# Kernel tuning notes

Measured on AMD Instinct MI355X. Metric: run time of the kernel, lower is better.

## Reference

```python
import jax, jax.numpy as jnp
import numpy as np

ITER = 6
GAMMA = 0.99
Q = 0.95


def _maxpool(x, win, stride, pad):
    # NCHW max pool
    return jax.lax.reduce_window(
        x, -jnp.inf, jax.lax.max,
        (1, 1, win, win), (1, 1, stride, stride),
        ((0, 0), (0, 0), (pad, pad), (pad, pad)))


def _nearest(x, size):
    # torch F.interpolate(mode='nearest'): src = floor(dst * in / out)
    H, W = size
    h_in, w_in = x.shape[2], x.shape[3]
    ih = (jnp.arange(H) * h_in) // H
    iw = (jnp.arange(W) * w_in) // W
    return x[:, :, ih[:, None], iw[None, :]]


def setup_inputs() -> dict:
    key = jax.random.key(0)
    ks = jax.random.split(key, 4)
    C, mid = 256, 16  # mid = int(sqrt(C))
    x = jax.random.normal(ks[0], (16, C, 128, 128), jnp.float32)
    w1 = jax.random.normal(ks[1], (mid, C), jnp.float32) / np.sqrt(C)
    b1 = jnp.zeros((mid,), jnp.float32)
    w2 = jax.random.normal(ks[2], (C, mid), jnp.float32) / np.sqrt(mid)
    b2 = jnp.zeros((C,), jnp.float32)
    return {"x": x, "w1": w1, "b1": b1, "w2": w2, "b2": b2}


def reference(x, w1, b1, w2, b2):
    B, C, H, W = x.shape
    # --- quantile activation mask (detached) ---
    flat = x.reshape(B, C, H * W)
    thr = jnp.quantile(flat, Q, axis=-1)[:, :, None, None]  # [B,C,1,1]
    M = jax.lax.stop_gradient((x >= thr).astype(x.dtype))
    # --- propagate field ---
    feat = x * M
    out = feat
    for i in range(ITER):
        g = jnp.asarray(GAMMA ** (2 ** i), x.dtype)
        if i == 0:
            feat = _maxpool(feat, 3, 1, 1) * g  # same-resolution 3x3 pool
            out = jnp.maximum(out, feat)
        else:
            # 5x5 stride-2 pool -> scale -> nearest upsample back to (H,W)
            feat = _nearest(_maxpool(feat, 5, 2, 2) * g, (H, W))
            out = jnp.maximum(out, feat)
    # --- receptor modulator: 1x1 conv -> relu -> 1x1 conv -> sigmoid ---
    h = jax.nn.relu(jnp.einsum('bchw,mc->bmhw', out, w1) + b1[None, :, None, None])
    R = jax.nn.sigmoid(jnp.einsum('bmhw,cm->bchw', h, w2) + b2[None, :, None, None])
    y = x * R
    return y
```

## Files before the change

kernel.cpp:

```cpp
#include <hip/hip_runtime.h>
#include <cmath>
#include <cfloat>

#define HW_ 16384

__device__ __forceinline__ unsigned f2key(float f){
    unsigned u = __float_as_uint(f);
    return u ^ ((u & 0x80000000u) ? 0xFFFFFFFFu : 0x80000000u);
}
__device__ __forceinline__ float key2f(unsigned k){
    unsigned u = (k & 0x80000000u) ? (k ^ 0x80000000u) : ~k;
    return __uint_as_float(u);
}
__device__ __forceinline__ unsigned short f2bf(float f){
    unsigned u = __float_as_uint(f);
    unsigned r = u + 0x7FFFu + ((u >> 16) & 1u);
    return (unsigned short)(r >> 16);
}
__device__ __forceinline__ float bf2f(unsigned short s){
    return __uint_as_float((unsigned)s << 16);
}
__device__ __forceinline__ unsigned pkmax(unsigned a, unsigned b){
    unsigned d;
    asm("v_pk_max_u16 %0, %1, %2" : "=v"(d) : "v"(a), "v"(b));
    return d;
}
__device__ __forceinline__ unsigned alignb(unsigned hi, unsigned lo){
    unsigned d;
    asm("v_alignbit_b32 %0, %1, %2, 16" : "=v"(d) : "v"(hi), "v"(lo));
    return d;
}
__device__ __forceinline__ unsigned cvtpk(float lo, float hi){
    unsigned d;
    asm("v_cvt_pk_bf16_f32 %0, %1, %2" : "=v"(d) : "v"(lo), "v"(hi));
    return d;
}
__device__ __forceinline__ unsigned wscan_incl(unsigned v, int lane){
    #pragma unroll
    for (int o = 1; o < 64; o <<= 1){
        unsigned u = __shfl_up(v, o);
        v += (lane >= o) ? u : 0u;
    }
    return v;
}

typedef short bf16x8 __attribute__((ext_vector_type(8)));
typedef float f32x4  __attribute__((ext_vector_type(4)));
__device__ __forceinline__ bf16x8 tofrag(uint4 q){
    union { uint4 q; bf16x8 f; } u; u.q = q; return u.f;
}

__global__ __launch_bounds__(256) void k0_split(
    const float* __restrict__ w1, const float* __restrict__ w2,
    unsigned short* __restrict__ W1h, unsigned short* __restrict__ W1l,
    unsigned short* __restrict__ W2h, unsigned short* __restrict__ W2l)
{
    int e = blockIdx.x * 256 + threadIdx.x;
    if (e < 4096){
        float f = w1[e];
        unsigned short hi = f2bf(f);
        W1h[e] = hi;
        W1l[e] = f2bf(f - bf2f(hi));
    } else {
        int e2 = e - 4096;
        float f = w2[e2];
        unsigned short hi = f2bf(f);
        W2h[e2] = hi;
        W2l[e2] = f2bf(f - bf2f(hi));
    }
}

__global__ __launch_bounds__(512, 6) void k1f(
    const float* __restrict__ x,
    unsigned short* __restrict__ outp, unsigned short* __restrict__ m64g,
    float g1, float q2, float q3, float q4, float q5, float q6)
{
    __shared__ __align__(16) unsigned short C0[16384];
    __shared__ __align__(16) unsigned short H5s[8192];
    __shared__ unsigned hist[1024];
    __shared__ unsigned wsum[8];
    __shared__ unsigned redA[8], redB[8];
    __shared__ unsigned s_dA, s_dB, s_cloA, s_cloB, s_keyA, s_keyB;

    const int tid = threadIdx.x;
    const int lane = tid & 63;
    const int wid = tid >> 6;
    const unsigned bc = blockIdx.x;
    const float4* xp4 = (const float4*)(x + (size_t)bc * HW_);

    unsigned key[32];

    #pragma unroll
    for (int k = 0; k < 2; ++k) hist[tid + k * 512] = 0u;
    __syncthreads();
    #pragma unroll
    for (int k = 0; k < 8; ++k){
        float4 v = xp4[tid + k * 512];
        key[4*k+0] = f2key(v.x);
        key[4*k+1] = f2key(v.y);
        key[4*k+2] = f2key(v.z);
        key[4*k+3] = f2key(v.w);
        atomicAdd(&hist[key[4*k+0] >> 22], 1u);
        atomicAdd(&hist[key[4*k+1] >> 22], 1u);
        atomicAdd(&hist[key[4*k+2] >> 22], 1u);
        atomicAdd(&hist[key[4*k+3] >> 22], 1u);
    }
    __syncthreads();

    unsigned rA = 15563u, rB = 15564u;
    unsigned prefVal = 0u, prefMask = 0u;
    bool done = false;

    {
        unsigned part = hist[tid*2] + hist[tid*2+1];
        unsigned incl = wscan_incl(part, lane);
        if (lane == 63) wsum[wid] = incl;
        __syncthreads();
        unsigned off = 0;
        #pragma unroll
        for (int w = 0; w < 8; ++w) off += (w < wid) ? wsum[w] : 0u;
        unsigned phi = incl + off;
        unsigned plo = phi - part;
        if (rA >= plo && rA < phi){
            unsigned c = plo;
            #pragma unroll
            for (int k = 0; k < 2; ++k){
                unsigned hh = hist[tid*2+k];
                if (rA < c + hh){ s_dA = tid*2+k; s_cloA = c; break; }
                c += hh;
            }
        }
        if (rB >= plo && rB < phi){
            unsigned c = plo;
            #pragma unroll
            for (int k = 0; k < 2; ++k){
                unsigned hh = hist[tid*2+k];
                if (rB < c + hh){ s_dB = tid*2+k; s_cloB = c; break; }
                c += hh;
            }
        }
        __syncthreads();
        unsigned dA = s_dA, dB = s_dB;
        if (dA != dB){
            unsigned locA = 0u, locB = 0xFFFFFFFFu;
            #pragma unroll
            for (int e = 0; e < 32; ++e){
                unsigned d = key[e] >> 22;
                if (d == dA) locA = max(locA, key[e]);
                if (d == dB) locB = min(locB, key[e]);
            }
            #pragma unroll
            for (int o = 32; o > 0; o >>= 1){
                locA = max(locA, __shfl_down(locA, o));
                locB = min(locB, __shfl_down(locB, o));
            }
            if (lane == 0){ redA[wid] = locA; redB[wid] = locB; }
            __syncthreads();
            if (tid == 0){
                unsigned a = redA[0], b = redB[0];
                for (int w = 1; w < 8; ++w){ a = max(a, redA[w]); b = min(b, redB[w]); }
                s_keyA = a; s_keyB = b;
            }
            __syncthreads();
            done = true;
        } else {
            prefVal = dA << 22; prefMask = 0x3FFu << 22;
            rA -= s_cloA; rB -= s_cloB;
            __syncthreads();
        }
    }

    if (!done){
        const int shifts[3] = {14, 6, 0};
        const int bitsv[3]  = {8, 8, 6};
        for (int lvl = 0; lvl < 3 && !done; ++lvl){
            int shift = shifts[lvl];
            unsigned nb = 1u << bitsv[lvl];
            unsigned msk = nb - 1u;
            if (tid < (int)nb) hist[tid] = 0u;
            __syncthreads();
            #pragma unroll
            for (int e = 0; e < 32; ++e){
                if ((key[e] & prefMask) == prefVal)
                    atomicAdd(&hist[(key[e] >> shift) & msk], 1u);
            }
            __syncthreads();
            unsigned part = (tid < (int)nb) ? hist[tid] : 0u;
            unsigned incl = wscan_incl(part, lane);
            if (lane == 63) wsum[wid] = incl;
            __syncthreads();
            unsigned off = 0;
            #pragma unroll
            for (int w = 0; w < 8; ++w) off += (w < wid) ? wsum[w] : 0u;
            unsigned phi = incl + off;
            unsigned plo = phi - part;
            if (tid < (int)nb){
                if (rA >= plo && rA < phi){ s_dA = tid; s_cloA = plo; }
                if (rB >= plo && rB < phi){ s_dB = tid; s_cloB = plo; }
            }
            __syncthreads();
            unsigned dA = s_dA, dB = s_dB;
            if (dA != dB){
                unsigned mA = prefMask | (msk << shift);
                unsigned vAp = prefVal | (dA << shift);
                unsigned vBp = prefVal | (dB << shift);
                unsigned locA = 0u, locB = 0xFFFFFFFFu;
                #pragma unroll
                for (int e = 0; e < 32; ++e){
                    if ((key[e] & mA) == vAp) locA = max(locA, key[e]);
                    if ((key[e] & mA) == vBp) locB = min(locB, key[e]);
                }
                #pragma unroll
                for (int o = 32; o > 0; o >>= 1){
                    locA = max(locA, __shfl_down(locA, o));
                    locB = min(locB, __shfl_down(locB, o));
                }
                if (lane == 0){ redA[wid] = locA; redB[wid] = locB; }
                __syncthreads();
                if (tid == 0){
                    unsigned a = redA[0], b = redB[0];
                    for (int w = 1; w < 8; ++w){ a = max(a, redA[w]); b = min(b, redB[w]); }
                    s_keyA = a; s_keyB = b;
                }
                __syncthreads();
                done = true;
            } else {
                prefVal |= dA << shift;
                prefMask |= msk << shift;
                rA -= s_cloA; rB -= s_cloB;
                if (lvl == 2){
                    if (tid == 0){ s_keyA = prefVal; s_keyB = prefVal; }
                    done = true;
                }
                __syncthreads();
            }
        }
    }

    float vlo = key2f(s_keyA);
    float vhi = key2f(s_keyB);
    float idxq = 0.95f * 16383.0f;
    float frac = idxq - floorf(idxq);
    const float thr = vlo * (1.0f - frac) + vhi * frac;

    #pragma unroll
    for (int k = 0; k < 8; ++k){
        int i = tid + k * 512;
        float f0 = key2f(key[4*k+0]); f0 = (f0 >= thr) ? f0 : 0.0f;
        float f1 = key2f(key[4*k+1]); f1 = (f1 >= thr) ? f1 : 0.0f;
        float f2 = key2f(key[4*k+2]); f2 = (f2 >= thr) ? f2 : 0.0f;
        float f3 = key2f(key[4*k+3]); f3 = (f3 >= thr) ? f3 : 0.0f;
        uint2 w; w.x = cvtpk(f0, f1); w.y = cvtpk(f2, f3);
        ((uint2*)C0)[i] = w;
    }
    __syncthreads();

    {
        const unsigned* C0w = (const unsigned*)C0;
        unsigned* outp32 = (unsigned*)(outp + (size_t)bc * HW_);
        const int wc = lane;
        const int r0 = wid * 16;

        unsigned hmA, hmB, hmC, cB, cC;
        {
            int r = r0 - 1;
            if (r < 0){ hmA = 0u; }
            else {
                unsigned w = C0w[r*64 + wc];
                unsigned wl = __shfl_up(w, 1);
                unsigned wr = __shfl_down(w, 1);
                if (wc == 0)  wl = 0u;
                if (wc == 63) wr = 0u;
                hmA = pkmax(pkmax(alignb(w, wl), w), alignb(wr, w));
            }
        }
        {
            int r = r0;
            unsigned w = C0w[r*64 + wc];
            unsigned wl = __shfl_up(w, 1);
            unsigned wr = __shfl_down(w, 1);
            if (wc == 0)  wl = 0u;
            if (wc == 63) wr = 0u;
            hmB = pkmax(pkmax(alignb(w, wl), w), alignb(wr, w));
            cB = w;
        }
        #pragma unroll
        for (int rr = 0; rr < 16; ++rr){
            int r = r0 + rr;
            {
                int rn = r + 1;
                if (rn > 127){ hmC = 0u; cC = 0u; }
                else {
                    unsigned w = C0w[rn*64 + wc];
                    unsigned wl = __shfl_up(w, 1);
                    unsigned wr = __shfl_down(w, 1);
                    if (wc == 0)  wl = 0u;
                    if (wc == 63) wr = 0u;
                    hmC = pkmax(pkmax(alignb(w, wl), w), alignb(wr, w));
                    cC = w;
                }
            }
            unsigned p1 = pkmax(pkmax(hmA, hmB), hmC);
            float a0 = g1 * bf2f((unsigned short)(p1 & 0xFFFFu));
            float a1v = g1 * bf2f((unsigned short)(p1 >> 16));
            outp32[r*64 + wc] = pkmax(cB, cvtpk(a0, a1v));
            unsigned wjm1 = __shfl_up(p1, 1);
            unsigned wjp1 = __shfl_down(p1, 1);
            if (wc == 0)  wjm1 = 0u;
            if (wc == 63) wjp1 = 0u;
            unsigned s = pkmax(wjm1, p1);
            s = pkmax(s, s >> 16);
            s = pkmax(s, wjp1 & 0xFFFFu);
            H5s[r*64 + wc] = (unsigned short)s;
            hmA = hmB; hmB = hmC; cB = cC;
        }
    }
    __syncthreads();

    unsigned* U = (unsigned*)C0;
    unsigned* T = ((unsigned*)C0) + 2048;
    float mf[8];
    #pragma unroll
    for (int k = 0; k < 4; ++k){
        int q = tid + k * 512;
        int i = q >> 5, wj = q & 31;
        int rr = 2 * i;
        const unsigned* H5w = (const unsigned*)H5s;
        unsigned m = pkmax(H5w[rr*32 + wj], H5w[(rr+1)*32 + wj]);
        if (rr >= 1) m = pkmax(m, H5w[(rr-1)*32 + wj]);
        if (rr >= 2) m = pkmax(m, H5w[(rr-2)*32 + wj]);
        if (rr + 2 <= 127) m = pkmax(m, H5w[(rr+2)*32 + wj]);
        U[q] = m;
        mf[2*k]   = q2 * bf2f((unsigned short)(m & 0xFFFFu));
        mf[2*k+1] = q2 * bf2f((unsigned short)(m >> 16));
    }
    __syncthreads();

    const float gs[4] = {q3, q4, q5, q6};
    #pragma unroll
    for (int it = 0; it < 4; ++it){
        #pragma unroll
        for (int k = 0; k < 4; ++k){
            int q = tid + k * 512;
            unsigned w = U[q];
            unsigned wl = __shfl_up(w, 1);
            unsigned wr = __shfl_down(w, 1);
            if ((q & 31) == 0)  wl = 0u;
            if ((q & 31) == 31) wr = 0u;
            T[q] = pkmax(pkmax(alignb(w, wl), w), alignb(wr, w));
        }
        __syncthreads();
        #pragma unroll
        for (int k = 0; k < 4; ++k){
            int q = tid + k * 512;
            int r = q >> 5;
            unsigned w = T[q];
            if (r > 0)  w = pkmax(w, T[q - 32]);
            if (r < 63) w = pkmax(w, T[q + 32]);
            U[q] = w;
            mf[2*k]   = fmaxf(mf[2*k],   gs[it] * bf2f((unsigned short)(w & 0xFFFFu)));
            mf[2*k+1] = fmaxf(mf[2*k+1], gs[it] * bf2f((unsigned short)(w >> 16)));
        }
        __syncthreads();
    }

    {
        unsigned* mp = (unsigned*)(m64g + (size_t)bc * 4096);
        #pragma unroll
        for (int k = 0; k < 4; ++k){
            int q = tid + k * 512;
            mp[q] = cvtpk(mf[2*k], mf[2*k+1]);
        }
    }
}

__global__ __launch_bounds__(256) void k3_mfma(
    const float* __restrict__ x,
    const unsigned short* __restrict__ outp, const unsigned short* __restrict__ m64,
    const unsigned short* __restrict__ W1h, const unsigned short* __restrict__ W1l,
    const unsigned short* __restrict__ W2h, const unsigned short* __restrict__ W2l,
    const float* __restrict__ b1, const float* __restrict__ b2,
    float* __restrict__ y)
{
    __shared__ __align__(16) unsigned SOUT32[8192];
    __shared__ __align__(16) float HS[4*16*18];

    const int tid  = threadIdx.x;
    const int lane = tid & 63;
    const int wid  = tid >> 6;
    const int blk  = blockIdx.x;
    const int b    = blk >> 8;
    const int px0  = (blk & 255) * 64;

    {
        const int row = px0 >> 7;
        const int mibase = (row >> 1)*64 + ((px0 & 127) >> 1);
        const unsigned* op32 = (const unsigned*)(outp + (size_t)b*256*HW_);
        const unsigned short* mp = m64 + (size_t)b*256*4096;
        #pragma unroll
        for (int i = 0; i < 16; ++i){
            int u = i*256 + tid;
            int c4 = u >> 5, pxp = u & 31;
            int ch0 = 2*c4;
            unsigned wA = op32[ch0*(HW_/2) + px0/2 + pxp];
            unsigned wB = op32[(ch0+1)*(HW_/2) + px0/2 + pxp];
            unsigned mA = (unsigned)mp[ch0*4096 + mibase + pxp] * 0x10001u;
            unsigned mB = (unsigned)mp[(ch0+1)*4096 + mibase + pxp] * 0x10001u;
            unsigned va = pkmax(wA, mA);
            unsigned vb = pkmax(wB, mB);
            unsigned wpa = (va & 0xFFFFu) | (vb << 16);
            unsigned wpb = (va >> 16) | (vb & 0xFFFF0000u);
            int sw = (pxp & 7) << 2;
            SOUT32[(2*pxp)  *128 + (c4 ^ sw)] = wpa;
            SOUT32[(2*pxp+1)*128 + (c4 ^ sw)] = wpb;
        }
    }
    __syncthreads();

    const int nidx = lane & 15;
    const int kg   = lane >> 4;
    const int px_t = wid*16 + nidx;
    const int sxz  = ((px_t >> 1) & 7) << 2;

    f32x4 acc = {0.f, 0.f, 0.f, 0.f};
    #pragma unroll
    for (int ks = 0; ks < 8; ++ks){
        int w0 = (ks*16 + kg*4) ^ sxz;
        bf16x8 fb = tofrag(*(const uint4*)&SOUT32[px_t*128 + w0]);
        bf16x8 ah = tofrag(*(const uint4*)(W1h + nidx*256 + ks*32 + kg*8));
        bf16x8 al = tofrag(*(const uint4*)(W1l + nidx*256 + ks*32 + kg*8));
        acc = __builtin_amdgcn_mfma_f32_16x16x32_bf16(ah, fb, acc, 0, 0, 0);
        acc = __builtin_amdgcn_mfma_f32_16x16x32_bf16(al, fb, acc, 0, 0, 0);
    }
    #pragma unroll
    for (int i2 = 0; i2 < 4; ++i2){
        int mid = kg*4 + i2;
        float hv = fmaxf(acc[i2] + b1[mid], 0.0f);
        HS[(wid*16 + nidx)*18 + mid] = hv;
    }
    __syncthreads();

    bf16x8 bh = {0,0,0,0,0,0,0,0}, bl = {0,0,0,0,0,0,0,0};
    if (kg < 2){
        const float* hp = &HS[(wid*16 + nidx)*18 + kg*8];
        float f0 = hp[0], f1 = hp[1], f2 = hp[2], f3 = hp[3];
        float f4 = hp[4], f5 = hp[5], f6 = hp[6], f7 = hp[7];
        unsigned short h0 = f2bf(f0), h1 = f2bf(f1), h2 = f2bf(f2), h3 = f2bf(f3);
        unsigned short h4 = f2bf(f4), h5 = f2bf(f5), h6 = f2bf(f6), h7 = f2bf(f7);
        bh[0] = (short)h0; bh[1] = (short)h1; bh[2] = (short)h2; bh[3] = (short)h3;
        bh[4] = (short)h4; bh[5] = (short)h5; bh[6] = (short)h6; bh[7] = (short)h7;
        bl[0] = (short)f2bf(f0 - bf2f(h0)); bl[1] = (short)f2bf(f1 - bf2f(h1));
        bl[2] = (short)f2bf(f2 - bf2f(h2)); bl[3] = (short)f2bf(f3 - bf2f(h3));
        bl[4] = (short)f2bf(f4 - bf2f(h4)); bl[5] = (short)f2bf(f5 - bf2f(h5));
        bl[6] = (short)f2bf(f6 - bf2f(h6)); bl[7] = (short)f2bf(f7 - bf2f(h7));
    }

    #pragma unroll 4
    for (int t = 0; t < 16; ++t){
        bf16x8 a2h = {0,0,0,0,0,0,0,0}, a2l = {0,0,0,0,0,0,0,0};
        if (kg < 2){
            a2h = tofrag(*(const uint4*)(W2h + (t*16 + nidx)*16 + kg*8));
            a2l = tofrag(*(const uint4*)(W2l + (t*16 + nidx)*16 + kg*8));
        }
        f32x4 d2 = {0.f, 0.f, 0.f, 0.f};
        d2 = __builtin_amdgcn_mfma_f32_16x16x32_bf16(a2h, bh, d2, 0, 0, 0);
        d2 = __builtin_amdgcn_mfma_f32_16x16x32_bf16(a2l, bh, d2, 0, 0, 0);
        d2 = __builtin_amdgcn_mfma_f32_16x16x32_bf16(a2h, bl, d2, 0, 0, 0);
        #pragma unroll
        for (int i2 = 0; i2 < 4; ++i2){
            int ch = t*16 + kg*4 + i2;
            float logit = d2[i2] + b2[ch];
            float R = 1.0f / (1.0f + __expf(-logit));
            size_t gidx = ((size_t)(b*256 + ch))*HW_ + px0 + px_t;
            y[gidx] = x[gidx] * R;
        }
    }
}

extern "C" void kernel_launch(void* const* d_in, const int* in_sizes, int n_in,
                              void* d_out, int out_size, void* d_ws, size_t ws_size,
                              hipStream_t stream) {
    const float* x  = (const float*)d_in[0];
    const float* w1 = (const float*)d_in[1];
    const float* b1 = (const float*)d_in[2];
    const float* w2 = (const float*)d_in[3];
    const float* b2 = (const float*)d_in[4];
    float* y  = (float*)d_out;
    char* ws = (char*)d_ws;

    unsigned short* outp = (unsigned short*)ws;
    unsigned short* m64  = (unsigned short*)(ws + 134217728);
    unsigned short* W1h  = (unsigned short*)(ws + 167772160);
    unsigned short* W1l  = W1h + 4096;
    unsigned short* W2h  = W1h + 8192;
    unsigned short* W2l  = W1h + 12288;

    float g1 = 0.99f;
    float q2 = (float)std::pow(0.99, 3.0);
    float q3 = (float)std::pow(0.99, 7.0);
    float q4 = (float)std::pow(0.99, 15.0);
    float q5 = (float)std::pow(0.99, 31.0);
    float q6 = (float)std::pow(0.99, 63.0);

    k0_split<<<32, 256, 0, stream>>>(w1, w2, W1h, W1l, W2h, W2l);
    k1f<<<4096, 512, 0, stream>>>(x, outp, m64, g1, q2, q3, q4, q5, q6);
    k3_mfma<<<4096, 256, 0, stream>>>(x, outp, m64, W1h, W1l, W2h, W2l, b1, b2, y);
}
```

Baseline: 336.4 us.

## Swap MFMA operand roles in second GEMM and vectorize x/y epilogue via shuffles

Drops the shared-memory round trip and barrier used to hand the hidden activations to the second MFMA. The bf16 hi/lo parts are now built in registers, moved between lanes with shuffles, and used as the A operand, with W2 becoming the B operand. This transposes the output layout so each lane holds 4 consecutive pixels of one channel, which lets the epilogue read x and write y as float4 instead of scalar strided accesses. It also adds a min-blocks-per-CU occupancy hint of 5, which may limit registers per thread.

```diff
diff --git a/kernel.cpp b/kernel.cpp
--- a/kernel.cpp
+++ b/kernel.cpp
@@ -374,7 +374,7 @@
     }
 }
 
-__global__ __launch_bounds__(256) void k3_mfma(
+__global__ __launch_bounds__(256, 5) void k3_mfma(
     const float* __restrict__ x,
     const unsigned short* __restrict__ outp, const unsigned short* __restrict__ m64,
     const unsigned short* __restrict__ W1h, const unsigned short* __restrict__ W1l,
@@ -383,7 +383,6 @@
     float* __restrict__ y)
 {
     __shared__ __align__(16) unsigned SOUT32[8192];
-    __shared__ __align__(16) float HS[4*16*18];
 
     const int tid  = threadIdx.x;
     const int lane = tid & 63;
@@ -432,48 +431,53 @@
         acc = __builtin_amdgcn_mfma_f32_16x16x32_bf16(ah, fb, acc, 0, 0, 0);
         acc = __builtin_amdgcn_mfma_f32_16x16x32_bf16(al, fb, acc, 0, 0, 0);
     }
-    #pragma unroll
-    for (int i2 = 0; i2 < 4; ++i2){
-        int mid = kg*4 + i2;
-        float hv = fmaxf(acc[i2] + b1[mid], 0.0f);
-        HS[(wid*16 + nidx)*18 + mid] = hv;
-    }
-    __syncthreads();
-
-    bf16x8 bh = {0,0,0,0,0,0,0,0}, bl = {0,0,0,0,0,0,0,0};
-    if (kg < 2){
-        const float* hp = &HS[(wid*16 + nidx)*18 + kg*8];
-        float f0 = hp[0], f1 = hp[1], f2 = hp[2], f3 = hp[3];
-        float f4 = hp[4], f5 = hp[5], f6 = hp[6], f7 = hp[7];
-        unsigned short h0 = f2bf(f0), h1 = f2bf(f1), h2 = f2bf(f2), h3 = f2bf(f3);
-        unsigned short h4 = f2bf(f4), h5 = f2bf(f5), h6 = f2bf(f6), h7 = f2bf(f7);
-        bh[0] = (short)h0; bh[1] = (short)h1; bh[2] = (short)h2; bh[3] = (short)h3;
-        bh[4] = (short)h4; bh[5] = (short)h5; bh[6] = (short)h6; bh[7] = (short)h7;
-        bl[0] = (short)f2bf(f0 - bf2f(h0)); bl[1] = (short)f2bf(f1 - bf2f(h1));
-        bl[2] = (short)f2bf(f2 - bf2f(h2)); bl[3] = (short)f2bf(f3 - bf2f(h3));
-        bl[4] = (short)f2bf(f4 - bf2f(h4)); bl[5] = (short)f2bf(f5 - bf2f(h5));
-        bl[6] = (short)f2bf(f6 - bf2f(h6)); bl[7] = (short)f2bf(f7 - bf2f(h7));
-    }
+
+    float h0 = fmaxf(acc[0] + b1[kg*4 + 0], 0.0f);
+    float h1 = fmaxf(acc[1] + b1[kg*4 + 1], 0.0f);
+    float h2 = fmaxf(acc[2] + b1[kg*4 + 2], 0.0f);
+    float h3 = fmaxf(acc[3] + b1[kg*4 + 3], 0.0f);
+    unsigned short e0 = f2bf(h0), e1 = f2bf(h1), e2 = f2bf(h2), e3 = f2bf(h3);
+    unsigned Wh0 = (unsigned)e0 | ((unsigned)e1 << 16);
+    unsigned Wh1 = (unsigned)e2 | ((unsigned)e3 << 16);
+    unsigned Wl0 = cvtpk(h0 - bf2f(e0), h1 - bf2f(e1));
+    unsigned Wl1 = cvtpk(h2 - bf2f(e2), h3 - bf2f(e3));
+
+    int s0 = ((kg & 1) << 5) + nidx;
+    int s1 = s0 + 16;
+    unsigned ah0 = (unsigned)__shfl((int)Wh0, s0);
+    unsigned ah1 = (unsigned)__shfl((int)Wh1, s0);
+    unsigned ah2 = (unsigned)__shfl((int)Wh0, s1);
+    unsigned ah3 = (unsigned)__shfl((int)Wh1, s1);
+    unsigned bl0 = (unsigned)__shfl((int)Wl0, s0);
+    unsigned bl1 = (unsigned)__shfl((int)Wl1, s0);
+    unsigned bl2 = (unsigned)__shfl((int)Wl0, s1);
+    unsigned bl3 = (unsigned)__shfl((int)Wl1, s1);
+    const bool act = (kg < 2);
+    uint4 qah = act ? (uint4){ah0, ah1, ah2, ah3} : (uint4){0u,0u,0u,0u};
+    uint4 qal = act ? (uint4){bl0, bl1, bl2, bl3} : (uint4){0u,0u,0u,0u};
+    bf16x8 A2h = tofrag(qah), A2l = tofrag(qal);
 
     #pragma unroll 4
     for (int t = 0; t < 16; ++t){
-        bf16x8 a2h = {0,0,0,0,0,0,0,0}, a2l = {0,0,0,0,0,0,0,0};
-        if (kg < 2){
-            a2h = tofrag(*(const uint4*)(W2h + (t*16 + nidx)*16 + kg*8));
-            a2l = tofrag(*(const uint4*)(W2l + (t*16 + nidx)*16 + kg*8));
+        uint4 qbh = {0u,0u,0u,0u}, qbl = {0u,0u,0u,0u};
+        if (act){
+            qbh = *(const uint4*)(W2h + (t*16 + nidx)*16 + kg*8);
+            qbl = *(const uint4*)(W2l + (t*16 + nidx)*16 + kg*8);
         }
         f32x4 d2 = {0.f, 0.f, 0.f, 0.f};
-        d2 = __builtin_amdgcn_mfma_f32_16x16x32_bf16(a2h, bh, d2, 0, 0, 0);
-        d2 = __builtin_amdgcn_mfma_f32_16x16x32_bf16(a2l, bh, d2, 0, 0, 0);
-        d2 = __builtin_amdgcn_mfma_f32_16x16x32_bf16(a2h, bl, d2, 0, 0, 0);
-        #pragma unroll
-        for (int i2 = 0; i2 < 4; ++i2){
-            int ch = t*16 + kg*4 + i2;
-            float logit = d2[i2] + b2[ch];
-            float R = 1.0f / (1.0f + __expf(-logit));
-            size_t gidx = ((size_t)(b*256 + ch))*HW_ + px0 + px_t;
-            y[gidx] = x[gidx] * R;
-        }
+        d2 = __builtin_amdgcn_mfma_f32_16x16x32_bf16(A2h, tofrag(qbh), d2, 0, 0, 0);
+        d2 = __builtin_amdgcn_mfma_f32_16x16x32_bf16(A2l, tofrag(qbh), d2, 0, 0, 0);
+        d2 = __builtin_amdgcn_mfma_f32_16x16x32_bf16(A2h, tofrag(qbl), d2, 0, 0, 0);
+        int ch = t*16 + nidx;
+        float bias = b2[ch];
+        size_t rowbase = ((size_t)(b*256 + ch))*HW_ + px0 + wid*16 + kg*4;
+        float4 xv = *(const float4*)&x[rowbase];
+        float4 yv;
+        yv.x = xv.x * (1.0f / (1.0f + __expf(-(d2[0] + bias))));
+        yv.y = xv.y * (1.0f / (1.0f + __expf(-(d2[1] + bias))));
+        yv.z = xv.z * (1.0f / (1.0f + __expf(-(d2[2] + bias))));
+        yv.w = xv.w * (1.0f / (1.0f + __expf(-(d2[3] + bias))));
+        *(float4*)&y[rowbase] = yv;
     }
 }
 
```

Result: slower. 351.9 us (+4.6%).
